# Kernel tuning notes

Measured on AMD Instinct MI355X. Metric: run time of the kernel, lower is better.

Reference implementation:

```python
import jax, jax.numpy as jnp
import numpy as np

EPS = 1e-7  # K.epsilon()

_LC = np.zeros((3, 3, 3), np.float32)  # Levi-Civita for 1x1->1
_LC[0, 1, 2] = _LC[1, 2, 0] = _LC[2, 0, 1] = 1.0
_LC[0, 2, 1] = _LC[2, 1, 0] = _LC[1, 0, 2] = -1.0


def _ssp(x):
    # shifted softplus: log(0.5*exp(x)+0.5)
    return jnp.log(0.5 * jnp.exp(x) + 0.5)


def _radial(image, w1, b1, w2, b2):
    # Sequential([Dense(32), Dense(feat)]) -- linear Dense layers (no activation)
    return (image @ w1 + b1) @ w2 + b2  # (m, a, b, feat)


def setup_inputs() -> dict:
    key = jax.random.key(0)
    ks = jax.random.split(key, 16)
    M, A, RBF, F, SI, H = 4, 256, 64, 32, 32, 32
    inp = {}
    inp["image"] = jax.random.uniform(ks[0], (M, A, A, RBF), dtype=jnp.float32)
    inp["vectors"] = jax.random.normal(ks[1], (M, A, A, 3), dtype=jnp.float32)
    inp["feat0"] = jax.random.normal(ks[2], (M, A, F, 1), dtype=jnp.float32)
    inp["feat1"] = jax.random.normal(ks[3], (M, A, F, 3), dtype=jnp.float32)
    i = 4
    for rin in (0, 1):
        for fro in (0, 1):
            tag = f"{rin}{fro}"
            inp[f"w1_{tag}"] = jax.random.normal(ks[i], (RBF, H)) / np.sqrt(RBF).astype(np.float32)
            inp[f"b1_{tag}"] = jnp.zeros((H,), jnp.float32)
            i += 1
            inp[f"w2_{tag}"] = jax.random.normal(ks[i], (H, F)) / np.sqrt(np.float32(H))
            inp[f"b2_{tag}"] = jnp.zeros((F,), jnp.float32)
            i += 1
    inp["w_si0"] = jax.random.normal(ks[i], (SI, 2 * F)) / np.sqrt(np.float32(2 * F)); i += 1
    inp["w_si1"] = jax.random.normal(ks[i], (SI, 3 * F)) / np.sqrt(np.float32(3 * F)); i += 1
    inp["b_act0"] = jnp.zeros((SI,), jnp.float32)
    inp["b_act1"] = jnp.zeros((SI,), jnp.float32)
    return inp


def reference(image, vectors, feat0, feat1,
              w1_00, b1_00, w2_00, b2_00,
              w1_01, b1_01, w2_01, b2_01,
              w1_10, b1_10, w2_10, b2_10,
              w1_11, b1_11, w2_11, b2_11,
              w_si0, w_si1, b_act0, b_act1):
    # mask where |r_ab| < eps (self-pairs / padding)
    mask = (jnp.sqrt(jnp.sum(vectors * vectors, axis=-1)) < EPS)[..., None]  # (m,a,b,1)

    def filt0(w1, b1, w2, b2):
        return _radial(image, w1, b1, w2, b2)  # (m,a,b,F), implicit rep index of size 1

    def filt1(w1, b1, w2, b2):
        r = jnp.where(mask, 0.0, _radial(image, w1, b1, w2, b2))  # masked radial
        return vectors[:, :, :, None, :] * r[..., None]  # (m,a,b,F,3)

    f0_in0 = filt0(w1_00, b1_00, w2_00, b2_00)
    f1_in0 = filt1(w1_01, b1_01, w2_01, b2_01)
    f0_in1 = filt0(w1_10, b1_10, w2_10, b2_10)
    f1_in1 = filt1(w1_11, b1_11, w2_11, b2_11)

    # point convolution (sum over neighbor atoms b)
    out_0x0_0 = jnp.einsum('mabf,mbfj->mafj', f0_in0, feat0)   # (m,a,F,1)
    out_0x1_1 = jnp.einsum('mabfi,mbfj->mafi', f1_in0, feat0)  # (m,a,F,3)
    out_1x0_1 = jnp.einsum('mabf,mbfj->mafj', f0_in1, feat1)   # (m,a,F,3)
    cg0 = jnp.eye(3, dtype=image.dtype)[None]                  # (1,3,3): 1x1->0
    out_1x1_0 = jnp.einsum('ijk,mabfj,mbfk->mafi', cg0, f1_in1, feat1)  # (m,a,F,1)
    lc = jnp.asarray(_LC, image.dtype)                         # 1x1->1
    out_1x1_1 = jnp.einsum('ijk,mabfj,mbfk->mafi', lc, f1_in1, feat1)   # (m,a,F,3)

    # concat along channel dim per output RO
    cat0 = jnp.concatenate([out_0x0_0, out_1x1_0], axis=2)  # (m,a,2F,1)
    cat1 = jnp.concatenate([out_0x1_1, out_1x0_1, out_1x1_1], axis=2)  # (m,a,3F,3)

    # self-interaction: einsum('mafi,gf->maig') then transpose -> (m,a,g,i)
    si0 = jnp.einsum('mafi,gf->magi', cat0, w_si0)  # (m,a,SI,1)
    si1 = jnp.einsum('mafi,gf->magi', cat1, w_si1)  # (m,a,SI,3)

    # equivariant activation
    o0 = _ssp(si0 + b_act0[None, None, :, None])
    n1 = jnp.sqrt(jnp.maximum(jnp.sum(si1 * si1, axis=-1), EPS))  # norm_with_epsilon
    a1 = _ssp(n1 + b_act1)
    o1 = si1 * (a1 / n1)[..., None]
    return (o0, o1)
```

## Files before the change

### kernel.cpp

```cpp
#include <hip/hip_runtime.h>
#include <math.h>

#define M_ 4
#define A_ 256
#define RBF_ 64
#define F_ 32
#define H_ 32
#define SI_ 32
#define TF_ 128

typedef __attribute__((ext_vector_type(8))) short bf16x8;
typedef __attribute__((ext_vector_type(4))) float f32x4;
typedef __attribute__((ext_vector_type(3))) float f32x3;

__device__ __forceinline__ unsigned short f2bf(float f) {
  union { float f; unsigned u; } v; v.f = f;
  unsigned r = v.u + 0x7FFFu + ((v.u >> 16) & 1u);
  return (unsigned short)(r >> 16);
}

__device__ __forceinline__ unsigned pack2bf(float lo, float hi) {
  union { float f; unsigned u; } a, b; a.f = lo; b.f = hi;
  return __builtin_amdgcn_perm(b.u + 0x8000u, a.u + 0x8000u, 0x07060302u);
}

__device__ __forceinline__ float sspf(float x) {
  return fmaxf(x, 0.f) + log1pf(expf(-fabsf(x))) - 0.6931471805599453f;
}

__global__ __launch_bounds__(256) void combine_weights(
    const float* __restrict__ w1_00, const float* __restrict__ b1_00,
    const float* __restrict__ w2_00, const float* __restrict__ b2_00,
    const float* __restrict__ w1_01, const float* __restrict__ b1_01,
    const float* __restrict__ w2_01, const float* __restrict__ b2_01,
    const float* __restrict__ w1_10, const float* __restrict__ b1_10,
    const float* __restrict__ w2_10, const float* __restrict__ b2_10,
    const float* __restrict__ w1_11, const float* __restrict__ b1_11,
    const float* __restrict__ w2_11, const float* __restrict__ b2_11,
    unsigned short* __restrict__ wsT, float* __restrict__ bcw)
{
  const float* w1s[4] = {w1_00, w1_01, w1_10, w1_11};
  const float* b1s[4] = {b1_00, b1_01, b1_10, b1_11};
  const float* w2s[4] = {w2_00, w2_01, w2_10, w2_11};
  const float* b2s[4] = {b2_00, b2_01, b2_10, b2_11};
  int tid = blockIdx.x * 256 + threadIdx.x;
  int k   = tid >> 7;
  int tf  = tid & 127;
  int tag = tf >> 5, f = tf & 31;
  const float* w1 = w1s[tag];
  const float* w2 = w2s[tag];
  float s = 0.f;
  for (int h = 0; h < H_; ++h) s += w1[k * H_ + h] * w2[h * F_ + f];
  wsT[tf * 64 + k] = f2bf(s);
  if (tid < TF_) {
    const float* b1 = b1s[tag];
    const float* b2 = b2s[tag];
    float sb = b2[f];
    for (int h = 0; h < H_; ++h) sb += b1[h] * w2[h * F_ + f];
    bcw[tf] = sb;
  }
}

__global__ __launch_bounds__(512, 4) void conv_partial(
    const float* __restrict__ image, const float* __restrict__ vectors,
    const float* __restrict__ feat0, const float* __restrict__ feat1,
    const unsigned short* __restrict__ wsT, const float* __restrict__ bcw,
    float* __restrict__ part)
{
  __shared__ __align__(16) unsigned short sA[128 * 72];
  __shared__ float sV[128 * 3];

  const int t    = threadIdx.x;
  const int bid  = blockIdx.x;
  const int ma   = bid >> 1;
  const int half = bid & 1;
  const int m    = ma >> 8;
  const int l    = t & 63;
  const int n    = l & 15;
  const int quad = l >> 4;
  const int wu    = __builtin_amdgcn_readfirstlane(t >> 6);
  const int role  = (wu + ((bid & 3) << 1)) & 7;
  const int which = role & 1;
  const int tag   = role >> 1;
  const int ct    = tag * 2 + which;
  const int f     = which * 16 + n;

  const unsigned short* wr = wsT + (ct * 16 + n) * 64 + quad * 8;
  const bf16x8 w0 = *(const bf16x8*)(wr);
  const bf16x8 w1 = *(const bf16x8*)(wr + 32);
  const float  bc = bcw[ct * 16 + n];

  const float* imgH = image + ((size_t)ma * A_ + half * 128) * RBF_;
  #pragma unroll
  for (int i = 0; i < 2; ++i) {
    int g = t + 512 * i;
    int r = g >> 3, c8 = g & 7;
    const float* src = imgH + r * RBF_ + c8 * 8;
    float4 v0 = *(const float4*)(src);
    float4 v1 = *(const float4*)(src + 4);
    uint4 pk;
    pk.x = pack2bf(v0.x, v0.y);
    pk.y = pack2bf(v0.z, v0.w);
    pk.z = pack2bf(v1.x, v1.y);
    pk.w = pack2bf(v1.z, v1.w);
    *(uint4*)&sA[r * 72 + c8 * 8] = pk;
  }
  if (t < 384) sV[t] = vectors[((size_t)ma * A_ + half * 128) * 3 + t];

  const int b0q = half * 128 + quad * 4;
  const float* p0c = feat0 + (size_t)(m * A_ + b0q) * F_ + f;
  const float* p1c = feat1 + ((size_t)(m * A_ + b0q) * F_ + f) * 3;
  const float* svc = &sV[quad * 4 * 3];
  const unsigned short* aBc = &sA[n * 72 + quad * 8];

  float gx[2][4], gy[2][4], gz[2][4];
  float pA = 0.f, pB0 = 0.f, pB1 = 0.f, pB2 = 0.f;

#define PF(BUF) { \
    if (tag <= 1) { \
      _Pragma("unroll") \
      for (int r = 0; r < 4; ++r) gx[BUF][r] = p0c[r * F_]; \
    } else { \
      _Pragma("unroll") \
      for (int r = 0; r < 4; ++r) { \
        f32x3 v = *(const f32x3*)(p1c + r * (F_ * 3)); \
        gx[BUF][r] = v[0]; gy[BUF][r] = v[1]; gz[BUF][r] = v[2]; \
      } \
    } \
    p0c += 16 * F_; p1c += 16 * F_ * 3; }

#define BODY(AOFF, SOFF, GX, GY, GZ) { \
    const bf16x8 a0 = *(const bf16x8*)(aBc + (AOFF)); \
    const bf16x8 a1 = *(const bf16x8*)(aBc + (AOFF) + 32); \
    f32x4 acc = {bc, bc, bc, bc}; \
    acc = __builtin_amdgcn_mfma_f32_16x16x32_bf16(a0, w0, acc, 0, 0, 0); \
    acc = __builtin_amdgcn_mfma_f32_16x16x32_bf16(a1, w1, acc, 0, 0, 0); \
    if (tag == 0) {             \
      _Pragma("unroll") \
      for (int r = 0; r < 4; ++r) pA += acc[r] * GX[r]; \
    } else if (tag == 1) {      \
      _Pragma("unroll") \
      for (int r = 0; r < 4; ++r) { \
        const float s = acc[r] * GX[r]; \
        pB0 += svc[(SOFF) + r * 3 + 0] * s; \
        pB1 += svc[(SOFF) + r * 3 + 1] * s; \
        pB2 += svc[(SOFF) + r * 3 + 2] * s; \
      } \
    } else if (tag == 2) {      \
      _Pragma("unroll") \
      for (int r = 0; r < 4; ++r) { \
        const float Rr = acc[r]; \
        pB0 += Rr * GX[r]; pB1 += Rr * GY[r]; pB2 += Rr * GZ[r]; \
      } \
    } else {                    \
      _Pragma("unroll") \
      for (int r = 0; r < 4; ++r) { \
        const float Rr = acc[r]; \
        const float ax = GX[r], ay = GY[r], az = GZ[r]; \
        const float vx = svc[(SOFF) + r * 3 + 0]; \
        const float vy = svc[(SOFF) + r * 3 + 1]; \
        const float vz = svc[(SOFF) + r * 3 + 2]; \
        float d = vx * ax; d = fmaf(vy, ay, d); d = fmaf(vz, az, d); \
        pA = fmaf(Rr, d, pA); \
        float c0 = vy * az; c0 = fmaf(-vz, ay, c0); pB0 = fmaf(Rr, c0, pB0); \
        float c1 = vz * ax; c1 = fmaf(-vx, az, c1); pB1 = fmaf(Rr, c1, pB1); \
        float c2 = vx * ay; c2 = fmaf(-vy, ax, c2); pB2 = fmaf(Rr, c2, pB2); \
      } \
    } }

  PF(0)
  __syncthreads();

  #pragma unroll 1
  for (int it = 0; it < 4; ++it) {
    PF(1)
    BODY(0, 0, gx[0], gy[0], gz[0])
    if (it < 3) PF(0)
    BODY(1152, 48, gx[1], gy[1], gz[1])
    aBc += 2 * 1152;
    svc += 2 * 48;
  }

#define QRED(x) { x += __shfl_xor(x, 16); x += __shfl_xor(x, 32); }
  QRED(pA) QRED(pB0) QRED(pB1) QRED(pB2)
  if (quad == 0) {
    float* dst = part + ((size_t)ma * 2 + half) * 352;
    if (tag == 0) {
      dst[f] = pA;
    } else if (tag == 1) {
      f32x3 v = {pB0, pB1, pB2};
      *(f32x3*)&dst[64 + f * 3] = v;
    } else if (tag == 2) {
      f32x3 v = {pB0, pB1, pB2};
      *(f32x3*)&dst[160 + f * 3] = v;
    } else {
      dst[32 + f] = pA;
      f32x3 v = {pB0, pB1, pB2};
      *(f32x3*)&dst[256 + f * 3] = v;
    }
  }
}

__global__ __launch_bounds__(64) void si_epilogue(
    const float* __restrict__ part,
    const float* __restrict__ w_si0, const float* __restrict__ w_si1,
    const float* __restrict__ b_act0, const float* __restrict__ b_act1,
    float* __restrict__ out)
{
  __shared__ float cat[352];
  const int ma = blockIdx.x;
  const int t  = threadIdx.x;
  const float* pA = part + (size_t)ma * 704;
  const float* pB = pA + 352;
  for (int s = t; s < 352; s += 64) cat[s] = pA[s] + pB[s];
  __syncthreads();

  const int outBase = ma * SI_;
  if (t < 32) {
    const float* wr = w_si0 + t * 64;
    float s = 0.f;
    #pragma unroll 8
    for (int ff = 0; ff < 64; ++ff) s += cat[ff] * wr[ff];
    s += b_act0[t];
    out[outBase + t] = sspf(s);
  } else {
    int g = t - 32;
    const float* wr = w_si1 + g * 96;
    float s0 = 0.f, s1 = 0.f, s2 = 0.f;
    #pragma unroll 8
    for (int ff = 0; ff < 96; ++ff) {
      float wv = wr[ff];
      s0 += cat[64 + ff * 3 + 0] * wv;
      s1 += cat[64 + ff * 3 + 1] * wv;
      s2 += cat[64 + ff * 3 + 2] * wv;
    }
    float n2 = s0 * s0 + s1 * s1 + s2 * s2;
    float n1 = sqrtf(fmaxf(n2, 1e-7f));
    float a1 = sspf(n1 + b_act1[g]);
    float sc = a1 / n1;
    int ob = M_ * A_ * SI_ + (outBase + g) * 3;
    out[ob + 0] = s0 * sc;
    out[ob + 1] = s1 * sc;
    out[ob + 2] = s2 * sc;
  }
}

extern "C" void kernel_launch(void* const* d_in, const int* in_sizes, int n_in,
                              void* d_out, int out_size, void* d_ws, size_t ws_size,
                              hipStream_t stream) {
  const float* image   = (const float*)d_in[0];
  const float* vectors = (const float*)d_in[1];
  const float* feat0   = (const float*)d_in[2];
  const float* feat1   = (const float*)d_in[3];
  const float* w_si0   = (const float*)d_in[20];
  const float* w_si1   = (const float*)d_in[21];
  const float* b_act0  = (const float*)d_in[22];
  const float* b_act1  = (const float*)d_in[23];
  unsigned short* wsT = (unsigned short*)d_ws;
  float* bcw  = (float*)((char*)d_ws + 16384);
  float* part = (float*)((char*)d_ws + 32768);
  float* out  = (float*)d_out;

  combine_weights<<<32, 256, 0, stream>>>(
      (const float*)d_in[4],  (const float*)d_in[5],
      (const float*)d_in[6],  (const float*)d_in[7],
      (const float*)d_in[8],  (const float*)d_in[9],
      (const float*)d_in[10], (const float*)d_in[11],
      (const float*)d_in[12], (const float*)d_in[13],
      (const float*)d_in[14], (const float*)d_in[15],
      (const float*)d_in[16], (const float*)d_in[17],
      (const float*)d_in[18], (const float*)d_in[19],
      wsT, bcw);

  conv_partial<<<2 * M_ * A_, 512, 0, stream>>>(
      image, vectors, feat0, feat1, wsT, bcw, part);

  si_epilogue<<<M_ * A_, 64, 0, stream>>>(
      part, w_si0, w_si1, b_act0, b_act1, out);
}
```

Measured before the change: 164.5 us.

## Fuse conv and self-interaction epilogue into one kernel with double-buffered image staging

Each block now handles a full (m,a) row of 256 neighbours instead of half. The image is streamed in 32-row chunks through two LDS buffers, with register prefetch of the next chunk overlapping MFMA work. The self-interaction and activation epilogue runs in the same block from an LDS cat buffer, which removes the partial-sum workspace round trip and the third kernel launch. The trade-offs are half as many blocks, less parallelism per row, and more barriers per block.

Result: no change. 165.0 us (+0.3%).

```diff
diff --git a/kernel.cpp b/kernel.cpp
--- a/kernel.cpp
+++ b/kernel.cpp
@@ -61,25 +61,26 @@
   }
 }
 
-__global__ __launch_bounds__(512, 4) void conv_partial(
+__global__ __launch_bounds__(512, 4) void conv_fused(
     const float* __restrict__ image, const float* __restrict__ vectors,
     const float* __restrict__ feat0, const float* __restrict__ feat1,
     const unsigned short* __restrict__ wsT, const float* __restrict__ bcw,
-    float* __restrict__ part)
+    const float* __restrict__ w_si0, const float* __restrict__ w_si1,
+    const float* __restrict__ b_act0, const float* __restrict__ b_act1,
+    float* __restrict__ out)
 {
-  __shared__ __align__(16) unsigned short sA[128 * 72];
-  __shared__ float sV[128 * 3];
+  __shared__ __align__(16) unsigned short sA[2][32 * 72];
+  __shared__ float sV[A_ * 3];
+  __shared__ float cat[352];
 
   const int t    = threadIdx.x;
-  const int bid  = blockIdx.x;
-  const int ma   = bid >> 1;
-  const int half = bid & 1;
+  const int ma   = blockIdx.x;
   const int m    = ma >> 8;
   const int l    = t & 63;
   const int n    = l & 15;
   const int quad = l >> 4;
   const int wu    = __builtin_amdgcn_readfirstlane(t >> 6);
-  const int role  = (wu + ((bid & 3) << 1)) & 7;
+  const int role  = (wu + ((ma & 3) << 1)) & 7;
   const int which = role & 1;
   const int tag   = role >> 1;
   const int ct    = tag * 2 + which;
@@ -90,28 +91,28 @@
   const bf16x8 w1 = *(const bf16x8*)(wr + 32);
   const float  bc = bcw[ct * 16 + n];
 
-  const float* imgH = image + ((size_t)ma * A_ + half * 128) * RBF_;
-  #pragma unroll
-  for (int i = 0; i < 2; ++i) {
-    int g = t + 512 * i;
-    int r = g >> 3, c8 = g & 7;
-    const float* src = imgH + r * RBF_ + c8 * 8;
-    float4 v0 = *(const float4*)(src);
-    float4 v1 = *(const float4*)(src + 4);
-    uint4 pk;
-    pk.x = pack2bf(v0.x, v0.y);
-    pk.y = pack2bf(v0.z, v0.w);
-    pk.z = pack2bf(v1.x, v1.y);
-    pk.w = pack2bf(v1.z, v1.w);
-    *(uint4*)&sA[r * 72 + c8 * 8] = pk;
-  }
-  if (t < 384) sV[t] = vectors[((size_t)ma * A_ + half * 128) * 3 + t];
-
-  const int b0q = half * 128 + quad * 4;
+  const int srow = t >> 4;
+  const int scol = (t & 15) * 4;
+  const float* gsrc = image + (size_t)ma * (A_ * RBF_) + srow * RBF_ + scol;
+  unsigned short* sd0 = &sA[0][srow * 72 + scol];
+  unsigned short* sd1 = &sA[1][srow * 72 + scol];
+
+  float4 rE = *(const float4*)(gsrc);
+  float4 rO = *(const float4*)(gsrc + 2048);
+  gsrc += 4096;
+
+  {
+    const float* vsrc = vectors + (size_t)ma * (A_ * 3);
+    sV[t] = vsrc[t];
+    if (t < 256) sV[t + 512] = vsrc[t + 512];
+  }
+
+  const int b0q = quad * 4;
   const float* p0c = feat0 + (size_t)(m * A_ + b0q) * F_ + f;
   const float* p1c = feat1 + ((size_t)(m * A_ + b0q) * F_ + f) * 3;
-  const float* svc = &sV[quad * 4 * 3];
-  const unsigned short* aBc = &sA[n * 72 + quad * 8];
+  const float* svc = &sV[b0q * 3];
+  const unsigned short* aB0 = &sA[0][n * 72 + quad * 8];
+  const unsigned short* aB1 = &sA[1][n * 72 + quad * 8];
 
   float gx[2][4], gy[2][4], gz[2][4];
   float pA = 0.f, pB0 = 0.f, pB1 = 0.f, pB2 = 0.f;
@@ -129,9 +130,9 @@
     } \
     p0c += 16 * F_; p1c += 16 * F_ * 3; }
 
-#define BODY(AOFF, SOFF, GX, GY, GZ) { \
-    const bf16x8 a0 = *(const bf16x8*)(aBc + (AOFF)); \
-    const bf16x8 a1 = *(const bf16x8*)(aBc + (AOFF) + 32); \
+#define BODY(AB, AOFF, SOFF, GX, GY, GZ) { \
+    const bf16x8 a0 = *(const bf16x8*)(AB + (AOFF)); \
+    const bf16x8 a1 = *(const bf16x8*)(AB + (AOFF) + 32); \
     f32x4 acc = {bc, bc, bc, bc}; \
     acc = __builtin_amdgcn_mfma_f32_16x16x32_bf16(a0, w0, acc, 0, 0, 0); \
     acc = __builtin_amdgcn_mfma_f32_16x16x32_bf16(a1, w1, acc, 0, 0, 0); \
@@ -168,80 +169,88 @@
       } \
     } }
 
+#define BARRIER() { \
+    asm volatile("s_waitcnt lgkmcnt(0)" ::: "memory"); \
+    __builtin_amdgcn_s_barrier(); \
+    asm volatile("" ::: "memory"); }
+
   PF(0)
-  __syncthreads();
+  { uint2 pk; pk.x = pack2bf(rE.x, rE.y); pk.y = pack2bf(rE.z, rE.w);
+    *(uint2*)sd0 = pk; }
+  BARRIER();
 
   #pragma unroll 1
-  for (int it = 0; it < 4; ++it) {
+  for (int d = 0; d < 4; ++d) {
+    if (d < 3) rE = *(const float4*)(gsrc);
     PF(1)
-    BODY(0, 0, gx[0], gy[0], gz[0])
-    if (it < 3) PF(0)
-    BODY(1152, 48, gx[1], gy[1], gz[1])
-    aBc += 2 * 1152;
-    svc += 2 * 48;
+    BODY(aB0, 0, 0, gx[0], gy[0], gz[0])
+    PF(0)
+    BODY(aB0, 1152, 48, gx[1], gy[1], gz[1])
+    { uint2 pk; pk.x = pack2bf(rO.x, rO.y); pk.y = pack2bf(rO.z, rO.w);
+      *(uint2*)sd1 = pk; }
+    BARRIER();
+    if (d < 3) rO = *(const float4*)(gsrc + 2048);
+    PF(1)
+    BODY(aB1, 0, 96, gx[0], gy[0], gz[0])
+    if (d < 3) PF(0)
+    BODY(aB1, 1152, 144, gx[1], gy[1], gz[1])
+    if (d < 3) {
+      uint2 pk; pk.x = pack2bf(rE.x, rE.y); pk.y = pack2bf(rE.z, rE.w);
+      *(uint2*)sd0 = pk;
+      BARRIER();
+    }
+    gsrc += 4096;
+    svc  += 192;
   }
 
 #define QRED(x) { x += __shfl_xor(x, 16); x += __shfl_xor(x, 32); }
   QRED(pA) QRED(pB0) QRED(pB1) QRED(pB2)
   if (quad == 0) {
-    float* dst = part + ((size_t)ma * 2 + half) * 352;
     if (tag == 0) {
-      dst[f] = pA;
+      cat[f] = pA;
     } else if (tag == 1) {
-      f32x3 v = {pB0, pB1, pB2};
-      *(f32x3*)&dst[64 + f * 3] = v;
+      cat[64 + f * 3 + 0] = pB0; cat[64 + f * 3 + 1] = pB1; cat[64 + f * 3 + 2] = pB2;
     } else if (tag == 2) {
-      f32x3 v = {pB0, pB1, pB2};
-      *(f32x3*)&dst[160 + f * 3] = v;
+      cat[160 + f * 3 + 0] = pB0; cat[160 + f * 3 + 1] = pB1; cat[160 + f * 3 + 2] = pB2;
     } else {
-      dst[32 + f] = pA;
-      f32x3 v = {pB0, pB1, pB2};
-      *(f32x3*)&dst[256 + f * 3] = v;
-    }
-  }
-}
-
-__global__ __launch_bounds__(64) void si_epilogue(
-    const float* __restrict__ part,
-    const float* __restrict__ w_si0, const float* __restrict__ w_si1,
-    const float* __restrict__ b_act0, const float* __restrict__ b_act1,
-    float* __restrict__ out)
-{
-  __shared__ float cat[352];
-  const int ma = blockIdx.x;
-  const int t  = threadIdx.x;
-  const float* pA = part + (size_t)ma * 704;
-  const float* pB = pA + 352;
-  for (int s = t; s < 352; s += 64) cat[s] = pA[s] + pB[s];
+      cat[32 + f] = pA;
+      cat[256 + f * 3 + 0] = pB0; cat[256 + f * 3 + 1] = pB1; cat[256 + f * 3 + 2] = pB2;
+    }
+  }
   __syncthreads();
 
-  const int outBase = ma * SI_;
-  if (t < 32) {
-    const float* wr = w_si0 + t * 64;
+  if (t < 256) {
+    const int g = t >> 3, p = t & 7;
+    const float* wrow = w_si1 + g * 96 + p * 12;
+    const float* c1 = &cat[64 + p * 36];
+    float s0 = 0.f, s1 = 0.f, s2 = 0.f;
+    #pragma unroll
+    for (int k = 0; k < 12; ++k) {
+      const float wv = wrow[k];
+      s0 = fmaf(c1[k * 3 + 0], wv, s0);
+      s1 = fmaf(c1[k * 3 + 1], wv, s1);
+      s2 = fmaf(c1[k * 3 + 2], wv, s2);
+    }
+    s0 += __shfl_xor(s0, 1); s0 += __shfl_xor(s0, 2); s0 += __shfl_xor(s0, 4);
+    s1 += __shfl_xor(s1, 1); s1 += __shfl_xor(s1, 2); s1 += __shfl_xor(s1, 4);
+    s2 += __shfl_xor(s2, 1); s2 += __shfl_xor(s2, 2); s2 += __shfl_xor(s2, 4);
+    if (p == 0) {
+      const float n2 = s0 * s0 + s1 * s1 + s2 * s2;
+      const float n1 = sqrtf(fmaxf(n2, 1e-7f));
+      const float a1 = sspf(n1 + b_act1[g]);
+      const float sc = a1 / n1;
+      const int ob = M_ * A_ * SI_ + (ma * SI_ + g) * 3;
+      out[ob + 0] = s0 * sc; out[ob + 1] = s1 * sc; out[ob + 2] = s2 * sc;
+    }
+  } else if (t < 320) {
+    const int t2 = t - 256, g = t2 >> 1, p = t2 & 1;
+    const float* wrow = w_si0 + g * 64 + p * 32;
+    const float* c0 = &cat[p * 32];
     float s = 0.f;
     #pragma unroll 8
-    for (int ff = 0; ff < 64; ++ff) s += cat[ff] * wr[ff];
-    s += b_act0[t];
-    out[outBase + t] = sspf(s);
-  } else {
-    int g = t - 32;
-    const float* wr = w_si1 + g * 96;
-    float s0 = 0.f, s1 = 0.f, s2 = 0.f;
-    #pragma unroll 8
-    for (int ff = 0; ff < 96; ++ff) {
-      float wv = wr[ff];
-      s0 += cat[64 + ff * 3 + 0] * wv;
-      s1 += cat[64 + ff * 3 + 1] * wv;
-      s2 += cat[64 + ff * 3 + 2] * wv;
-    }
-    float n2 = s0 * s0 + s1 * s1 + s2 * s2;
-    float n1 = sqrtf(fmaxf(n2, 1e-7f));
-    float a1 = sspf(n1 + b_act1[g]);
-    float sc = a1 / n1;
-    int ob = M_ * A_ * SI_ + (outBase + g) * 3;
-    out[ob + 0] = s0 * sc;
-    out[ob + 1] = s1 * sc;
-    out[ob + 2] = s2 * sc;
+    for (int k = 0; k < 32; ++k) s = fmaf(c0[k], wrow[k], s);
+    s += __shfl_xor(s, 1);
+    if (p == 0) out[ma * SI_ + g] = sspf(s + b_act0[g]);
   }
 }
 
@@ -258,7 +267,6 @@
   const float* b_act1  = (const float*)d_in[23];
   unsigned short* wsT = (unsigned short*)d_ws;
   float* bcw  = (float*)((char*)d_ws + 16384);
-  float* part = (float*)((char*)d_ws + 32768);
   float* out  = (float*)d_out;
 
   combine_weights<<<32, 256, 0, stream>>>(
@@ -272,9 +280,7 @@
       (const float*)d_in[18], (const float*)d_in[19],
       wsT, bcw);
 
-  conv_partial<<<2 * M_ * A_, 512, 0, stream>>>(
-      image, vectors, feat0, feat1, wsT, bcw, part);
-
-  si_epilogue<<<M_ * A_, 64, 0, stream>>>(
-      part, w_si0, w_si1, b_act0, b_act1, out);
-}
+  conv_fused<<<M_ * A_, 512, 0, stream>>>(
+      image, vectors, feat0, feat1, wsT, bcw,
+      w_si0, w_si1, b_act0, b_act1, out);
+}
```
